# Performance work log

Hardware: AMD Instinct MI355X
Metric: run time of the kernel (lower is better)

The kernel has to match this reference:

```python
import jax, jax.numpy as jnp
import numpy as np

B, T, E, H, L, V = 16, 512, 512, 8, 4, 2048
HS = E // H  # head_size = n_embd // n_head
FF = 4 * E


def _ln(x, g, b):
    m = x.mean(-1, keepdims=True)
    v = ((x - m) ** 2).mean(-1, keepdims=True)
    return (x - m) * jax.lax.rsqrt(v + 1e-5) * g + b


def setup_inputs() -> dict:
    key = jax.random.key(0)
    ks = jax.random.split(key, 16)
    s = jnp.float32(0.02)
    return {
        "idx": jax.random.randint(ks[0], (B, T), 0, V),
        "tok_emb": jax.random.normal(ks[1], (V, E), jnp.float32) * s,
        "pos_emb": jax.random.normal(ks[2], (T, E), jnp.float32) * s,
        "Wq": jax.random.normal(ks[3], (L, E, E), jnp.float32) * s,
        "Wk": jax.random.normal(ks[4], (L, E, E), jnp.float32) * s,
        "Wv": jax.random.normal(ks[5], (L, E, E), jnp.float32) * s,
        "rel": jax.random.normal(ks[6], (L, 2 * T - 1, HS), jnp.float32) * s,
        "Wo": jax.random.normal(ks[7], (L, E, E), jnp.float32) * s,
        "bo": jnp.zeros((L, E), jnp.float32),
        "ln1_g": jnp.ones((L, E), jnp.float32),
        "ln1_b": jnp.zeros((L, E), jnp.float32),
        "W1": jax.random.normal(ks[8], (L, E, FF), jnp.float32) * s,
        "b1": jnp.zeros((L, FF), jnp.float32),
        "W2": jax.random.normal(ks[9], (L, FF, E), jnp.float32) * s,
        "b2": jnp.zeros((L, E), jnp.float32),
        "ln2_g": jnp.ones((L, E), jnp.float32),
        "ln2_b": jnp.zeros((L, E), jnp.float32),
        "lnf_g": jnp.ones((E,), jnp.float32),
        "lnf_b": jnp.zeros((E,), jnp.float32),
        "Wlm": jax.random.normal(ks[10], (E, V), jnp.float32) * s,
        "blm": jnp.zeros((V,), jnp.float32),
    }


def reference(idx, tok_emb, pos_emb, Wq, Wk, Wv, rel, Wo, bo, ln1_g, ln1_b,
              W1, b1, W2, b2, ln2_g, ln2_b, lnf_g, lnf_b, Wlm, blm):
    x = tok_emb[idx] + pos_emb[None, :T]  # (B,T,E)
    ri = jnp.arange(T)
    rel_idx = ri[:, None] - ri[None, :] + (T - 1)  # block_size == T
    causal = ri[:, None] >= ri[None, :]            # (T,T) lower-triangular
    scale = jnp.float32(1.0 / np.sqrt(HS))
    for l in range(L):
        h = _ln(x, ln1_g[l], ln1_b[l])
        # NOTE: torch code does .view(B, H, T, HS) on a (B, T, H*HS) tensor
        # (NOT a transpose) -- jnp.reshape matches row-major view semantics.
        q = (h @ Wq[l]).reshape(B, H, T, HS)
        k = (h @ Wk[l]).reshape(B, H, T, HS)
        v = (h @ Wv[l]).reshape(B, H, T, HS)
        re = rel[l][rel_idx]  # (T,T,HS)
        # rel scores: sum_d q[b,h,i,d]*re[i,j,d]; avoid the 5D intermediate
        scores = jnp.einsum('bhid,bhjd->bhij', q, k) * scale \
               + jnp.einsum('bhid,ijd->bhij', q, re)
        scores = jnp.where(causal, scores, -jnp.inf)
        att = jax.nn.softmax(scores, axis=-1)  # dropout disabled (eval)
        ctx = jnp.einsum('bhij,bhjd->bhid', att, v)
        ctx = jnp.swapaxes(ctx, 1, 2).reshape(B, T, H * HS)
        x = x + ctx @ Wo[l] + bo[l]
        h2 = _ln(x, ln2_g[l], ln2_b[l])
        x = x + jax.nn.relu(h2 @ W1[l] + b1[l]) @ W2[l] + b2[l]
    x = _ln(x, lnf_g, lnf_b)
    return x @ Wlm + blm  # logits (B,T,V)
```

## Files before the change

kernel.cpp:

```cpp
#include <hip/hip_runtime.h>
#include <hip/hip_bf16.h>
#include <stdint.h>

typedef __hip_bfloat16 bf16;
typedef __attribute__((ext_vector_type(8))) short bf16x8;
typedef __attribute__((ext_vector_type(8))) short short8;
typedef __attribute__((ext_vector_type(4))) float f32x4;

#define DEV __device__ __forceinline__

static constexpr int Bn = 16, Tn = 512, En = 512, Hn = 8, Ln = 4, Vn = 2048;
static constexpr int HSn = 64, FFn = 2048, Mn = Bn * Tn;
static constexpr int SQ = 1536;

DEV f32x4 mfma16(bf16x8 a, bf16x8 b, f32x4 c) {
  return __builtin_amdgcn_mfma_f32_16x16x32_bf16(a, b, c, 0, 0, 0);
}
DEV float b2f(bf16 x) { return __bfloat162float(x); }
DEV bf16 f2b(float x) { return __float2bfloat16(x); }
DEV short f2s(float x) { bf16 h = f2b(x); return reinterpret_cast<short&>(h); }

DEV void gload16(const void* g, void* l) {
  __builtin_amdgcn_global_load_lds(
      (const __attribute__((address_space(1))) void*)(uintptr_t)g,
      (__attribute__((address_space(3))) void*)(uint32_t)(uintptr_t)l, 16, 0, 0);
}

__global__ __launch_bounds__(256) void ktranspose(const float* __restrict__ in,
                                                  bf16* __restrict__ out, int R, int C,
                                                  long in_zs, long out_zs) {
  __shared__ float tile[32][33];
  int z = blockIdx.z;
  const float* inz = in + (size_t)z * in_zs;
  bf16* outz = out + (size_t)z * out_zs;
  int c0 = blockIdx.x * 32, r0 = blockIdx.y * 32;
  for (int k = 0; k < 32; k += 8)
    tile[threadIdx.y + k][threadIdx.x] =
        inz[(size_t)(r0 + threadIdx.y + k) * C + (c0 + threadIdx.x)];
  __syncthreads();
  for (int k = 0; k < 32; k += 8)
    outz[(size_t)(c0 + threadIdx.y + k) * R + (r0 + threadIdx.x)] =
        f2b(tile[threadIdx.x][threadIdx.y + k]);
}

__global__ __launch_bounds__(256) void kcast(const float* __restrict__ in,
                                             bf16* __restrict__ out, int n) {
  int i = blockIdx.x * 256 + threadIdx.x;
  if (i < n) out[i] = f2b(in[i]);
}

__global__ __launch_bounds__(256) void kembed(const int* __restrict__ idx,
                                              const float* __restrict__ tok,
                                              const float* __restrict__ pos,
                                              float* __restrict__ x) {
  int i = blockIdx.x * 256 + threadIdx.x;
  int e4 = (i & 127) * 4;
  int bt = i >> 7;
  int t = bt & (Tn - 1);
  f32x4 tv = *(const f32x4*)(tok + (size_t)idx[bt] * En + e4);
  f32x4 pv = *(const f32x4*)(pos + (size_t)t * En + e4);
  *(f32x4*)(x + (size_t)bt * En + e4) = tv + pv;
}

__global__ __launch_bounds__(256) void kln(const float* __restrict__ x,
                                           const float* __restrict__ g,
                                           const float* __restrict__ b,
                                           bf16* __restrict__ out) {
  int row = blockIdx.x * 4 + (threadIdx.x >> 6);
  int lane = threadIdx.x & 63;
  const float* xr = x + (size_t)row * En + lane * 8;
  f32x4 a0 = *(const f32x4*)xr;
  f32x4 a1 = *(const f32x4*)(xr + 4);
  float s = a0[0] + a0[1] + a0[2] + a0[3] + a1[0] + a1[1] + a1[2] + a1[3];
  for (int m = 1; m < 64; m <<= 1) s += __shfl_xor(s, m);
  float mean = s * (1.f / En);
  float s2 = 0.f;
  for (int j = 0; j < 4; j++) { float d0 = a0[j] - mean, d1 = a1[j] - mean; s2 += d0 * d0 + d1 * d1; }
  for (int m = 1; m < 64; m <<= 1) s2 += __shfl_xor(s2, m);
  float rstd = rsqrtf(s2 * (1.f / En) + 1e-5f);
  f32x4 g0 = *(const f32x4*)(g + lane * 8), g1 = *(const f32x4*)(g + lane * 8 + 4);
  f32x4 b0 = *(const f32x4*)(b + lane * 8), b1 = *(const f32x4*)(b + lane * 8 + 4);
  short8 ov;
  for (int j = 0; j < 4; j++) {
    ov[j] = f2s((a0[j] - mean) * rstd * g0[j] + b0[j]);
    ov[j + 4] = f2s((a1[j] - mean) * rstd * g1[j] + b1[j]);
  }
  *(short8*)(out + (size_t)row * En + lane * 8) = ov;
}

template <int BM, int BN, int TW, int DB, int SWZ, int NBIAS, int RELU, int MODE>
__global__ __launch_bounds__(TW) void kgemm(const bf16* __restrict__ A,
                                            const bf16* __restrict__ Bt,
                                            const float* __restrict__ bias,
                                            float* __restrict__ outf,
                                            bf16* __restrict__ outh, int Ndim, int K) {
  constexpr int NW = TW / 64;
  constexpr int WCN = NW / 2;
  constexpr int WM = BM / 2, WN = BN / WCN, MI = WM / 16, NI = WN / 16;
  constexpr int NB = DB ? 2 : 1;
  __shared__ bf16 As[NB][BM * 64];
  __shared__ bf16 Bs[NB][BN * 64];
  int t = threadIdx.x, lane = t & 63, w = t >> 6;
  int lr = lane & 15, lg = lane >> 4;
  int sx = lr & 7;
  int wr = w / WCN, wc = w % WCN;
  int bx, by;
  if (SWZ) {
    int id = blockIdx.x + gridDim.x * blockIdx.y;
    int xcd = id & 7, s = id >> 3;
    int gx = gridDim.x;
    by = xcd * 8 + s / gx;
    bx = s % gx;
  } else {
    bx = blockIdx.x; by = blockIdx.y;
  }
  int br = by * BM, bc = bx * BN;
  f32x4 acc[MI][NI] = {};
  int rl = lane >> 3, cb = (lane & 7) ^ rl;
  const bf16* Abase = A + (size_t)(br + w * (BM / NW) + rl) * K + cb * 8;
  const bf16* Bbase = Bt + (size_t)(bc + w * (BN / NW) + rl) * K + cb * 8;

  auto STAGE = [&](int buf, int kt) {
    for (int c = 0; c < BM / (8 * NW); c++)
      gload16(Abase + (size_t)(c * 8) * K + kt, &As[buf][(w * (BM / NW) + c * 8) * 64]);
    for (int c = 0; c < BN / (8 * NW); c++)
      gload16(Bbase + (size_t)(c * 8) * K + kt, &Bs[buf][(w * (BN / NW) + c * 8) * 64]);
  };
  auto COMPUTE = [&](int buf) {
    for (int kk = 0; kk < 2; kk++) {
      int gb = (kk * 4 + lg) ^ sx;
      bf16x8 af[MI], bfr[NI];
      for (int mi = 0; mi < MI; mi++)
        af[mi] = *(const bf16x8*)&As[buf][(wr * WM + mi * 16 + lr) * 64 + gb * 8];
      for (int ni = 0; ni < NI; ni++)
        bfr[ni] = *(const bf16x8*)&Bs[buf][(wc * WN + ni * 16 + lr) * 64 + gb * 8];
      for (int mi = 0; mi < MI; mi++)
        for (int ni = 0; ni < NI; ni++)
          acc[mi][ni] = mfma16(af[mi], bfr[ni], acc[mi][ni]);
    }
  };

  if (DB) {
    STAGE(0, 0);
    __syncthreads();
    int nt = K / 64;
    for (int t2 = 0; t2 < nt; t2++) {
      int cur = t2 & 1;
      if (t2 + 1 < nt) STAGE(cur ^ 1, (t2 + 1) * 64);
      COMPUTE(cur);
      __syncthreads();
    }
  } else {
    for (int kt = 0; kt < K; kt += 64) {
      __syncthreads();
      STAGE(0, kt);
      __syncthreads();
      COMPUTE(0);
    }
  }

  for (int mi = 0; mi < MI; mi++)
    for (int ni = 0; ni < NI; ni++)
      for (int r = 0; r < 4; r++) {
        int row = br + wr * WM + mi * 16 + lg * 4 + r;
        int col = bc + wc * WN + ni * 16 + lr;
        float val = acc[mi][ni][r];
        if (NBIAS) val += bias[col];
        if (RELU) val = fmaxf(val, 0.f);
        if (MODE == 1) outf[(size_t)row * Ndim + col] += val;
        else if (MODE == 2) outf[(size_t)row * Ndim + col] = val;
        else outh[(size_t)row * Ndim + col] = f2b(val);
      }
}

__global__ __launch_bounds__(256) void kattn(const bf16* __restrict__ qkv,
                                             const bf16* __restrict__ rel,
                                             bf16* __restrict__ ctx) {
  __shared__ bf16 Ks[64 * 64];
  __shared__ bf16 Vs[64 * 64];
  __shared__ bf16 Prel[4][16 * 81];
  __shared__ bf16 Ps[4][16 * 64];
  int pairp = blockIdx.x, bh = blockIdx.y;
  int b = bh >> 3, hh = bh & 7;
  int t = threadIdx.x, lane = t & 63, w = t >> 6;
  int lr = lane & 15, lg = lane >> 4;
  int sx = lr & 7;
  int rl8 = lane >> 3, cbk = (lane & 7) ^ rl8;
  const size_t headrow = (size_t)(b * Tn + hh * 64);
  bf16* prw = &Prel[w][0];
  bf16* psw = &Ps[w][0];
  int jp = t >> 3, db = (t & 7) * 8;

  for (int ph = 0; ph < 2; ph++) {
    int iblk = ph ? (7 - pairp) : pairp;
    int i0w = iblk * 64 + w * 16;
    bf16x8 aq[2];
    {
      int t2 = i0w + lr;
      const bf16* qp = qkv + (headrow + (t2 >> 3)) * SQ + (t2 & 7) * 64;
      aq[0] = *(const bf16x8*)(qp + lg * 8);
      aq[1] = *(const bf16x8*)(qp + 32 + lg * 8);
    }
    f32x4 o[4] = {};
    float m_run = -3e38f, l_run = 0.f;

    for (int jb = 0; jb <= iblk * 64; jb += 64) {
      bool diag = (jb == iblk * 64);
      int j0 = jb + jp * 2;
      bf16x8 va = *(const bf16x8*)(qkv + (headrow + (j0 >> 3)) * SQ + (j0 & 7) * 64 + 1024 + db);
      bf16x8 vb2 = *(const bf16x8*)(qkv + (headrow + ((j0 + 1) >> 3)) * SQ + ((j0 + 1) & 7) * 64 + 1024 + db);
      __syncthreads();
      for (int c = 0; c < 2; c++) {
        int row = w * 16 + c * 8 + rl8;
        const bf16* src = qkv + (headrow + ((jb + row) >> 3)) * SQ +
                          (row & 7) * 64 + 512 + cbk * 8;
        gload16(src, &Ks[(w * 16 + c * 8) * 64]);
      }
      {
        const short* pa = (const short*)&va;
        const short* pb = (const short*)&vb2;
        for (int u = 0; u < 8; u++) {
          int d = db + u;
          int idx = d * 64 + (((jp >> 2) ^ (d & 7)) * 8) + (jp & 3) * 2;
          uint32_t pk = (uint32_t)(uint16_t)pa[u] | ((uint32_t)(uint16_t)pb[u] << 16);
          *(uint32_t*)((short*)Vs + idx) = pk;
        }
      }
      __syncthreads();
      int njmax = diag ? w : 3;
      int nmmin = diag ? 3 - w : 0;
      __builtin_amdgcn_s_setprio(1);
      f32x4 sqk[4] = {};
      for (int nj = 0; nj <= njmax; nj++) {
        int row = nj * 16 + lr;
        bf16x8 kb0 = *(const bf16x8*)&Ks[row * 64 + ((lg ^ sx) * 8)];
        bf16x8 kb1 = *(const bf16x8*)&Ks[row * 64 + (((4 + lg) ^ sx) * 8)];
        sqk[nj] = mfma16(kb0, aq[0], sqk[nj]);
        sqk[nj] = mfma16(kb1, aq[1], sqk[nj]);
      }
      int base = i0w - jb + 448;
      for (int nm = nmmin; nm < 5; nm++) {
        int mrow = base + nm * 16 + lr;
        if (mrow > 1022) mrow = 1022;
        const bf16* rp = rel + (size_t)mrow * 64;
        f32x4 sr = {};
        sr = mfma16(aq[0], *(const bf16x8*)(rp + lg * 8), sr);
        sr = mfma16(aq[1], *(const bf16x8*)(rp + 32 + lg * 8), sr);
        for (int r = 0; r < 4; r++)
          prw[(lg * 4 + r) * 81 + nm * 16 + lr] = f2b(sr[r]);
      }
      __builtin_amdgcn_s_setprio(0);
      float sv[4][4];
      for (int nj = 0; nj < 4; nj++)
        for (int r = 0; r < 4; r++) sv[nj][r] = -3e38f;
      float mloc = -3e38f;
      for (int nj = 0; nj <= njmax; nj++)
        for (int r = 0; r < 4; r++) {
          int jj = nj * 16 + lg * 4 + r;
          float val = sqk[nj][r] * 0.125f + b2f(prw[lr * 81 + (lr - jj + 63)]);
          if (jb + jj > i0w + lr) val = -3e38f;
          sv[nj][r] = val;
          mloc = fmaxf(mloc, val);
        }
      mloc = fmaxf(mloc, __shfl_xor(mloc, 16));
      mloc = fmaxf(mloc, __shfl_xor(mloc, 32));
      float mnew = fmaxf(m_run, mloc);
      float corr = __expf(m_run - mnew);
      m_run = mnew;
      float lsum = 0.f;
      for (int nj = 0; nj < 4; nj++)
        for (int r = 0; r < 4; r++) {
          float p = __expf(sv[nj][r] - mnew);
          lsum += p;
          psw[lr * 64 + (((nj * 2 + (lg >> 1)) ^ sx) * 8) + (lg & 1) * 4 + r] = f2b(p);
        }
      lsum += __shfl_xor(lsum, 16);
      lsum += __shfl_xor(lsum, 32);
      l_run = l_run * corr + lsum;
      for (int r = 0; r < 4; r++) {
        float c = __shfl(corr, lg * 4 + r);
        for (int nd = 0; nd < 4; nd++) o[nd][r] *= c;
      }
      __builtin_amdgcn_s_setprio(1);
      bf16x8 ap0 = *(const bf16x8*)&psw[lr * 64 + ((lg ^ sx) * 8)];
      bf16x8 ap1 = *(const bf16x8*)&psw[lr * 64 + (((4 + lg) ^ sx) * 8)];
      for (int nd = 0; nd < 4; nd++) {
        int d = nd * 16 + lr;
        bf16x8 vb0 = *(const bf16x8*)&Vs[d * 64 + ((lg ^ sx) * 8)];
        bf16x8 vb1 = *(const bf16x8*)&Vs[d * 64 + (((4 + lg) ^ sx) * 8)];
        o[nd] = mfma16(ap0, vb0, o[nd]);
        o[nd] = mfma16(ap1, vb1, o[nd]);
      }
      __builtin_amdgcn_s_setprio(0);
    }
    for (int r = 0; r < 4; r++) {
      float linv = 1.f / __shfl(l_run, lg * 4 + r);
      int row = i0w + lg * 4 + r;
      for (int nd = 0; nd < 4; nd++)
        ctx[((size_t)b * Tn + row) * En + hh * 64 + nd * 16 + lr] = f2b(o[nd][r] * linv);
    }
  }
}

extern "C" void kernel_launch(void* const* d_in, const int* in_sizes, int n_in,
                              void* d_out, int out_size, void* d_ws, size_t ws_size,
                              hipStream_t stream) {
  (void)in_sizes; (void)n_in; (void)out_size; (void)ws_size;
  const int* idx = (const int*)d_in[0];
  const float* tok = (const float*)d_in[1];
  const float* pos = (const float*)d_in[2];
  const float* Wq = (const float*)d_in[3];
  const float* Wk = (const float*)d_in[4];
  const float* Wv = (const float*)d_in[5];
  const float* rel = (const float*)d_in[6];
  const float* Wo = (const float*)d_in[7];
  const float* bo = (const float*)d_in[8];
  const float* ln1_g = (const float*)d_in[9];
  const float* ln1_b = (const float*)d_in[10];
  const float* W1 = (const float*)d_in[11];
  const float* b1 = (const float*)d_in[12];
  const float* W2 = (const float*)d_in[13];
  const float* b2 = (const float*)d_in[14];
  const float* ln2_g = (const float*)d_in[15];
  const float* ln2_b = (const float*)d_in[16];
  const float* lnf_g = (const float*)d_in[17];
  const float* lnf_b = (const float*)d_in[18];
  const float* Wlm = (const float*)d_in[19];
  const float* blm = (const float*)d_in[20];

  char* ws = (char*)d_ws;
  float* x = (float*)(ws + 0);
  bf16* h = (bf16*)(ws + 16777216);
  bf16* qkv = (bf16*)(ws + 25165824);
  bf16* ctx = (bf16*)(ws + 50331648);
  bf16* ffn1 = qkv;
  bf16* wqkvT = (bf16*)(ws + 58720256);
  bf16* woT = wqkvT + (size_t)Ln * SQ * En;
  bf16* w1T = woT + (size_t)Ln * En * En;
  bf16* w2T = w1T + (size_t)Ln * En * FFn;
  bf16* wlmT = w2T + (size_t)Ln * FFn * En;
  bf16* relc = wlmT + (size_t)En * Vn;
  float* outf = (float*)d_out;

  dim3 tb(32, 8);
  ktranspose<<<dim3(16, 16, Ln), tb, 0, stream>>>(Wq, wqkvT, En, En, (long)En * En, (long)SQ * En);
  ktranspose<<<dim3(16, 16, Ln), tb, 0, stream>>>(Wk, wqkvT + 512 * 512, En, En, (long)En * En, (long)SQ * En);
  ktranspose<<<dim3(16, 16, Ln), tb, 0, stream>>>(Wv, wqkvT + 2 * 512 * 512, En, En, (long)En * En, (long)SQ * En);
  ktranspose<<<dim3(16, 16, Ln), tb, 0, stream>>>(Wo, woT, En, En, (long)En * En, (long)En * En);
  ktranspose<<<dim3(64, 16, Ln), tb, 0, stream>>>(W1, w1T, En, FFn, (long)En * FFn, (long)En * FFn);
  ktranspose<<<dim3(16, 64, Ln), tb, 0, stream>>>(W2, w2T, FFn, En, (long)FFn * En, (long)FFn * En);
  ktranspose<<<dim3(64, 16, 1), tb, 0, stream>>>(Wlm, wlmT, En, Vn, 0, 0);
  kcast<<<(Ln * (2 * Tn - 1) * HSn + 255) / 256, 256, 0, stream>>>(
      rel, relc, Ln * (2 * Tn - 1) * HSn);

  kembed<<<(Mn * En / 4) / 256, 256, 0, stream>>>(idx, tok, pos, x);

  for (int l = 0; l < Ln; l++) {
    kln<<<Mn / 4, 256, 0, stream>>>(x, ln1_g + (size_t)l * En, ln1_b + (size_t)l * En, h);
    kgemm<128, 128, 256, 0, 1, 0, 0, 0><<<dim3(12, 64), 256, 0, stream>>>(
        h, wqkvT + (size_t)l * SQ * En, nullptr, nullptr, qkv, SQ, En);
    kattn<<<dim3(4, 128), 256, 0, stream>>>(
        qkv, relc + (size_t)l * (2 * Tn - 1) * HSn, ctx);
    kgemm<128, 128, 512, 1, 1, 1, 0, 1><<<dim3(4, 64), 512, 0, stream>>>(
        ctx, woT + (size_t)l * En * En, bo + (size_t)l * En, x, nullptr, En, En);
    kln<<<Mn / 4, 256, 0, stream>>>(x, ln2_g + (size_t)l * En, ln2_b + (size_t)l * En, h);
    kgemm<128, 128, 256, 0, 1, 1, 1, 0><<<dim3(16, 64), 256, 0, stream>>>(
        h, w1T + (size_t)l * En * FFn, b1 + (size_t)l * FFn, nullptr, ffn1, FFn, En);
    kgemm<128, 128, 512, 1, 1, 1, 0, 1><<<dim3(4, 64), 512, 0, stream>>>(
        ffn1, w2T + (size_t)l * FFn * En, b2 + (size_t)l * En, x, nullptr, En, FFn);
  }
  kln<<<Mn / 4, 256, 0, stream>>>(x, lnf_g, lnf_b, h);
  kgemm<128, 128, 256, 0, 1, 1, 0, 2><<<dim3(16, 64), 256, 0, stream>>>(
      h, wlmT, blm, outf, nullptr, Vn, En);
}
```

Measured before the change: 660.9 us.

## Stage 128-key tiles in attention and use 512-thread GEMMs everywhere

The attention kernel now loads 128 keys and values per shared-memory stage and processes them as two 64-key sub-steps, halving the number of barrier pairs and global-load rounds per query block. The V transpose layout is widened to 128 columns with an adjusted swizzle. Separately, the QKV, FFN1 and LM-head GEMMs switch to the 512-thread template configuration that the other GEMMs already use. The trade-off is more shared memory per block, which may lower attention occupancy, plus wasted loads when the last tile extends past the causal diagonal.

```diff
diff --git a/kernel.cpp b/kernel.cpp
--- a/kernel.cpp
+++ b/kernel.cpp
@@ -176,8 +176,8 @@
 __global__ __launch_bounds__(256) void kattn(const bf16* __restrict__ qkv,
                                              const bf16* __restrict__ rel,
                                              bf16* __restrict__ ctx) {
-  __shared__ bf16 Ks[64 * 64];
-  __shared__ bf16 Vs[64 * 64];
+  __shared__ bf16 Ks[128 * 64];
+  __shared__ bf16 Vs[64 * 128];
   __shared__ bf16 Prel[4][16 * 81];
   __shared__ bf16 Ps[4][16 * 64];
   int pairp = blockIdx.x, bh = blockIdx.y;
@@ -203,95 +203,110 @@
     }
     f32x4 o[4] = {};
     float m_run = -3e38f, l_run = 0.f;
-
-    for (int jb = 0; jb <= iblk * 64; jb += 64) {
-      bool diag = (jb == iblk * 64);
-      int j0 = jb + jp * 2;
-      bf16x8 va = *(const bf16x8*)(qkv + (headrow + (j0 >> 3)) * SQ + (j0 & 7) * 64 + 1024 + db);
-      bf16x8 vb2 = *(const bf16x8*)(qkv + (headrow + ((j0 + 1) >> 3)) * SQ + ((j0 + 1) & 7) * 64 + 1024 + db);
-      __syncthreads();
-      for (int c = 0; c < 2; c++) {
-        int row = w * 16 + c * 8 + rl8;
-        const bf16* src = qkv + (headrow + ((jb + row) >> 3)) * SQ +
+    int ntiles = (iblk >> 1) + 1;
+
+    for (int jt = 0; jt < ntiles; jt++) {
+      int jbase = jt * 128;
+      bf16x8 vv[4];
+#pragma unroll
+      for (int u = 0; u < 4; u++) {
+        int j0 = jbase + jp * 4 + u;
+        vv[u] = *(const bf16x8*)(qkv + (headrow + (j0 >> 3)) * SQ + (j0 & 7) * 64 + 1024 + db);
+      }
+      __syncthreads();
+#pragma unroll
+      for (int c = 0; c < 4; c++) {
+        int row = w * 32 + c * 8 + rl8;
+        const bf16* src = qkv + (headrow + ((jbase + row) >> 3)) * SQ +
                           (row & 7) * 64 + 512 + cbk * 8;
-        gload16(src, &Ks[(w * 16 + c * 8) * 64]);
-      }
-      {
-        const short* pa = (const short*)&va;
-        const short* pb = (const short*)&vb2;
+        gload16(src, &Ks[(w * 32 + c * 8) * 64]);
+      }
+#pragma unroll
+      for (int pr = 0; pr < 2; pr++) {
+        const short* pa = (const short*)&vv[pr * 2];
+        const short* pb = (const short*)&vv[pr * 2 + 1];
+        int j0 = jp * 4 + pr * 2;
+        int jblk = j0 >> 3, jin = j0 & 7;
+#pragma unroll
         for (int u = 0; u < 8; u++) {
           int d = db + u;
-          int idx = d * 64 + (((jp >> 2) ^ (d & 7)) * 8) + (jp & 3) * 2;
+          int idx = d * 128 + ((jblk ^ (d & 7)) * 8) + jin;
           uint32_t pk = (uint32_t)(uint16_t)pa[u] | ((uint32_t)(uint16_t)pb[u] << 16);
           *(uint32_t*)((short*)Vs + idx) = pk;
         }
       }
       __syncthreads();
-      int njmax = diag ? w : 3;
-      int nmmin = diag ? 3 - w : 0;
-      __builtin_amdgcn_s_setprio(1);
-      f32x4 sqk[4] = {};
-      for (int nj = 0; nj <= njmax; nj++) {
-        int row = nj * 16 + lr;
-        bf16x8 kb0 = *(const bf16x8*)&Ks[row * 64 + ((lg ^ sx) * 8)];
-        bf16x8 kb1 = *(const bf16x8*)&Ks[row * 64 + (((4 + lg) ^ sx) * 8)];
-        sqk[nj] = mfma16(kb0, aq[0], sqk[nj]);
-        sqk[nj] = mfma16(kb1, aq[1], sqk[nj]);
-      }
-      int base = i0w - jb + 448;
-      for (int nm = nmmin; nm < 5; nm++) {
-        int mrow = base + nm * 16 + lr;
-        if (mrow > 1022) mrow = 1022;
-        const bf16* rp = rel + (size_t)mrow * 64;
-        f32x4 sr = {};
-        sr = mfma16(aq[0], *(const bf16x8*)(rp + lg * 8), sr);
-        sr = mfma16(aq[1], *(const bf16x8*)(rp + 32 + lg * 8), sr);
-        for (int r = 0; r < 4; r++)
-          prw[(lg * 4 + r) * 81 + nm * 16 + lr] = f2b(sr[r]);
-      }
-      __builtin_amdgcn_s_setprio(0);
-      float sv[4][4];
-      for (int nj = 0; nj < 4; nj++)
-        for (int r = 0; r < 4; r++) sv[nj][r] = -3e38f;
-      float mloc = -3e38f;
-      for (int nj = 0; nj <= njmax; nj++)
+#pragma unroll
+      for (int su = 0; su < 2; su++) {
+        int jb = jbase + su * 64;
+        if (jb > iblk * 64) break;
+        bool diag = (jb == iblk * 64);
+        int njmax = diag ? w : 3;
+        int nmmin = diag ? 3 - w : 0;
+        __builtin_amdgcn_s_setprio(1);
+        f32x4 sqk[4] = {};
+        for (int nj = 0; nj <= njmax; nj++) {
+          int row = su * 64 + nj * 16 + lr;
+          bf16x8 kb0 = *(const bf16x8*)&Ks[row * 64 + ((lg ^ sx) * 8)];
+          bf16x8 kb1 = *(const bf16x8*)&Ks[row * 64 + (((4 + lg) ^ sx) * 8)];
+          sqk[nj] = mfma16(kb0, aq[0], sqk[nj]);
+          sqk[nj] = mfma16(kb1, aq[1], sqk[nj]);
+        }
+        int base = i0w - jb + 448;
+        for (int nm = nmmin; nm < 5; nm++) {
+          int mrow = base + nm * 16 + lr;
+          if (mrow > 1022) mrow = 1022;
+          const bf16* rp = rel + (size_t)mrow * 64;
+          f32x4 sr = {};
+          sr = mfma16(aq[0], *(const bf16x8*)(rp + lg * 8), sr);
+          sr = mfma16(aq[1], *(const bf16x8*)(rp + 32 + lg * 8), sr);
+          for (int r = 0; r < 4; r++)
+            prw[(lg * 4 + r) * 81 + nm * 16 + lr] = f2b(sr[r]);
+        }
+        __builtin_amdgcn_s_setprio(0);
+        float sv[4][4];
+        for (int nj = 0; nj < 4; nj++)
+          for (int r = 0; r < 4; r++) sv[nj][r] = -3e38f;
+        float mloc = -3e38f;
+        for (int nj = 0; nj <= njmax; nj++)
+          for (int r = 0; r < 4; r++) {
+            int jj = nj * 16 + lg * 4 + r;
+            float val = sqk[nj][r] * 0.125f + b2f(prw[lr * 81 + (lr - jj + 63)]);
+            if (jb + jj > i0w + lr) val = -3e38f;
+            sv[nj][r] = val;
+            mloc = fmaxf(mloc, val);
+          }
+        mloc = fmaxf(mloc, __shfl_xor(mloc, 16));
+        mloc = fmaxf(mloc, __shfl_xor(mloc, 32));
+        float mnew = fmaxf(m_run, mloc);
+        float corr = __expf(m_run - mnew);
+        m_run = mnew;
+        float lsum = 0.f;
+        for (int nj = 0; nj < 4; nj++)
+          for (int r = 0; r < 4; r++) {
+            float p = __expf(sv[nj][r] - mnew);
+            lsum += p;
+            psw[lr * 64 + (((nj * 2 + (lg >> 1)) ^ sx) * 8) + (lg & 1) * 4 + r] = f2b(p);
+          }
+        lsum += __shfl_xor(lsum, 16);
+        lsum += __shfl_xor(lsum, 32);
+        l_run = l_run * corr + lsum;
         for (int r = 0; r < 4; r++) {
-          int jj = nj * 16 + lg * 4 + r;
-          float val = sqk[nj][r] * 0.125f + b2f(prw[lr * 81 + (lr - jj + 63)]);
-          if (jb + jj > i0w + lr) val = -3e38f;
-          sv[nj][r] = val;
-          mloc = fmaxf(mloc, val);
-        }
-      mloc = fmaxf(mloc, __shfl_xor(mloc, 16));
-      mloc = fmaxf(mloc, __shfl_xor(mloc, 32));
-      float mnew = fmaxf(m_run, mloc);
-      float corr = __expf(m_run - mnew);
-      m_run = mnew;
-      float lsum = 0.f;
-      for (int nj = 0; nj < 4; nj++)
-        for (int r = 0; r < 4; r++) {
-          float p = __expf(sv[nj][r] - mnew);
-          lsum += p;
-          psw[lr * 64 + (((nj * 2 + (lg >> 1)) ^ sx) * 8) + (lg & 1) * 4 + r] = f2b(p);
-        }
-      lsum += __shfl_xor(lsum, 16);
-      lsum += __shfl_xor(lsum, 32);
-      l_run = l_run * corr + lsum;
-      for (int r = 0; r < 4; r++) {
-        float c = __shfl(corr, lg * 4 + r);
-        for (int nd = 0; nd < 4; nd++) o[nd][r] *= c;
-      }
-      __builtin_amdgcn_s_setprio(1);
-      bf16x8 ap0 = *(const bf16x8*)&psw[lr * 64 + ((lg ^ sx) * 8)];
-      bf16x8 ap1 = *(const bf16x8*)&psw[lr * 64 + (((4 + lg) ^ sx) * 8)];
-      for (int nd = 0; nd < 4; nd++) {
-        int d = nd * 16 + lr;
-        bf16x8 vb0 = *(const bf16x8*)&Vs[d * 64 + ((lg ^ sx) * 8)];
-        bf16x8 vb1 = *(const bf16x8*)&Vs[d * 64 + (((4 + lg) ^ sx) * 8)];
-        o[nd] = mfma16(ap0, vb0, o[nd]);
-        o[nd] = mfma16(ap1, vb1, o[nd]);
-      }
-      __builtin_amdgcn_s_setprio(0);
+          float c = __shfl(corr, lg * 4 + r);
+          for (int nd = 0; nd < 4; nd++) o[nd][r] *= c;
+        }
+        __builtin_amdgcn_s_setprio(1);
+        bf16x8 ap0 = *(const bf16x8*)&psw[lr * 64 + ((lg ^ sx) * 8)];
+        bf16x8 ap1 = *(const bf16x8*)&psw[lr * 64 + (((4 + lg) ^ sx) * 8)];
+        for (int nd = 0; nd < 4; nd++) {
+          int d = nd * 16 + lr;
+          bf16x8 vb0 = *(const bf16x8*)&Vs[d * 128 + ((su * 8 + (lg ^ sx)) * 8)];
+          bf16x8 vb1 = *(const bf16x8*)&Vs[d * 128 + ((su * 8 + ((4 + lg) ^ sx)) * 8)];
+          o[nd] = mfma16(ap0, vb0, o[nd]);
+          o[nd] = mfma16(ap1, vb1, o[nd]);
+        }
+        __builtin_amdgcn_s_setprio(0);
+      }
     }
     for (int r = 0; r < 4; r++) {
       float linv = 1.f / __shfl(l_run, lg * 4 + r);
@@ -357,19 +372,19 @@
 
   for (int l = 0; l < Ln; l++) {
     kln<<<Mn / 4, 256, 0, stream>>>(x, ln1_g + (size_t)l * En, ln1_b + (size_t)l * En, h);
-    kgemm<128, 128, 256, 0, 1, 0, 0, 0><<<dim3(12, 64), 256, 0, stream>>>(
+    kgemm<128, 128, 512, 1, 1, 0, 0, 0><<<dim3(12, 64), 512, 0, stream>>>(
         h, wqkvT + (size_t)l * SQ * En, nullptr, nullptr, qkv, SQ, En);
     kattn<<<dim3(4, 128), 256, 0, stream>>>(
         qkv, relc + (size_t)l * (2 * Tn - 1) * HSn, ctx);
     kgemm<128, 128, 512, 1, 1, 1, 0, 1><<<dim3(4, 64), 512, 0, stream>>>(
         ctx, woT + (size_t)l * En * En, bo + (size_t)l * En, x, nullptr, En, En);
     kln<<<Mn / 4, 256, 0, stream>>>(x, ln2_g + (size_t)l * En, ln2_b + (size_t)l * En, h);
-    kgemm<128, 128, 256, 0, 1, 1, 1, 0><<<dim3(16, 64), 256, 0, stream>>>(
+    kgemm<128, 128, 512, 1, 1, 1, 1, 0><<<dim3(16, 64), 512, 0, stream>>>(
         h, w1T + (size_t)l * En * FFn, b1 + (size_t)l * FFn, nullptr, ffn1, FFn, En);
     kgemm<128, 128, 512, 1, 1, 1, 0, 1><<<dim3(4, 64), 512, 0, stream>>>(
         ffn1, w2T + (size_t)l * FFn * En, b2 + (size_t)l * En, x, nullptr, En, FFn);
   }
   kln<<<Mn / 4, 256, 0, stream>>>(x, lnf_g, lnf_b, h);
-  kgemm<128, 128, 256, 0, 1, 1, 0, 2><<<dim3(16, 64), 256, 0, stream>>>(
+  kgemm<128, 128, 512, 1, 1, 1, 0, 2><<<dim3(16, 64), 512, 0, stream>>>(
       h, wlmT, blm, outf, nullptr, Vn, En);
 }
```

New measurement: 668.9 us. No clear change (+1.2%).
